# Optimization experiments

Hardware: AMD Instinct MI355X
Metric: run time of the kernel (lower is better)

The kernel has to match this reference:

```python
import jax, jax.numpy as jnp
import numpy as np

DIM = 512; E = 4; K = 4; R = 4; N = 1
B = 32; H = 14; W = 14; TOPK = 2; AUXW = 0.01

def _silu(x):
    return x * jax.nn.sigmoid(x)

def _ss2d(x, in_proj_w, conv_w, conv_b, x_proj_w, dt_proj_w, dt_proj_b, A_logs, Ds, norm_w, norm_b):
    # x: [B,H,W,dim]; single SS2D expert (ssm_ratio=1 -> d_inner=dim), no out_proj, with out_norm
    Bn, Hh, Ww, d = x.shape
    L = Hh * Ww
    xz = jnp.einsum('bhwc,oc->bhwo', x, in_proj_w)            # [B,H,W,2d]
    xp, z = jnp.split(xz, 2, axis=-1)
    xc = xp.transpose(0, 3, 1, 2)                              # [B,d,H,W]
    xc = jax.lax.conv_general_dilated(xc, conv_w, (1, 1), 'SAME', feature_group_count=d)
    xc = _silu(xc + conv_b[None, :, None, None])
    x_hw = xc.reshape(Bn, d, L)
    x_wh = xc.transpose(0, 1, 3, 2).reshape(Bn, d, L)
    # directions: h, h_flip, v, v_flip
    xs = jnp.stack([x_hw, jnp.flip(x_hw, -1), x_wh, jnp.flip(x_wh, -1)], axis=1)  # [B,K,d,L]
    x_dbl = jnp.einsum('bkdl,kcd->bkcl', xs, x_proj_w)         # [B,K,R+2N,L]
    dts = x_dbl[:, :, :R]
    Bs = x_dbl[:, :, R:R + N]                                  # [B,K,N,L]
    Cs = x_dbl[:, :, R + N:]                                   # [B,K,N,L]
    dts = jnp.einsum('bkrl,kdr->bkdl', dts, dt_proj_w)
    dts = jax.nn.softplus(dts + dt_proj_b[None, :, :, None])   # [B,K,d,L]
    A = -jnp.exp(A_logs).reshape(K, d, N)                      # [K,d,N]
    dA = jnp.exp(dts[..., None] * A[None, :, :, None, :])      # [B,K,d,L,N]
    dBu = (dts * xs)[..., None] * Bs.transpose(0, 1, 3, 2)[:, :, None]  # [B,K,d,L,N]
    dA_t = jnp.moveaxis(dA, 3, 0)                              # [L,B,K,d,N]
    dBu_t = jnp.moveaxis(dBu, 3, 0)
    h0 = jnp.zeros((Bn, K, d, N), dtype=x.dtype)
    def step(h, inp):
        a, bu = inp
        h = a * h + bu
        return h, h
    _, hs = jax.lax.scan(step, h0, (dA_t, dBu_t))              # [L,B,K,d,N]
    Cs_t = jnp.moveaxis(Cs, 3, 0)[:, :, :, None, :]            # [L,B,K,1,N]
    y = jnp.moveaxis((hs * Cs_t).sum(-1), 0, -1)               # [B,K,d,L]
    y = y + xs * Ds.reshape(K, d)[None, :, :, None]
    y0 = y[:, 0]
    y1 = jnp.flip(y[:, 1], -1)
    y2 = y[:, 2].reshape(Bn, d, Ww, Hh).transpose(0, 1, 3, 2).reshape(Bn, d, L)
    y3 = jnp.flip(y[:, 3], -1).reshape(Bn, d, Ww, Hh).transpose(0, 1, 3, 2).reshape(Bn, d, L)
    ys = (y0 + y1 + y2 + y3).transpose(0, 2, 1).reshape(Bn, Hh, Ww, d)
    mu = ys.mean(-1, keepdims=True)
    var = ys.var(-1, keepdims=True)
    ys = (ys - mu) * jax.lax.rsqrt(var + 1e-5) * norm_w + norm_b
    return ys * _silu(z)

def setup_inputs() -> dict:
    ks = jax.random.split(jax.random.key(0), 8)
    f = jnp.float32
    return {
        'x': jax.random.normal(ks[0], (B, H, W, DIM), dtype=f),
        'expert_queries': jax.random.normal(ks[1], (E, DIM), dtype=f) / jnp.sqrt(float(DIM)),
        'temperature': jnp.ones((1,), dtype=f),
        'in_proj_w': jax.random.normal(ks[2], (E, 2 * DIM, DIM), dtype=f) / jnp.sqrt(float(DIM)),
        'conv_w': jax.random.normal(ks[3], (E, DIM, 1, 3, 3), dtype=f) / 3.0,
        'conv_b': jnp.zeros((E, DIM), dtype=f),
        'x_proj_w': jax.random.normal(ks[4], (E, K, R + 2 * N, DIM), dtype=f) / jnp.sqrt(float(DIM)),
        'dt_proj_w': jax.random.normal(ks[5], (E, K, DIM, R), dtype=f) / jnp.sqrt(float(R)),
        'dt_proj_b': jnp.zeros((E, K, DIM), dtype=f),
        'A_logs': jax.random.uniform(ks[6], (E, K * DIM, N), dtype=f),
        'Ds': jnp.ones((E, K * DIM), dtype=f),
        'norm_w': jnp.ones((E, DIM), dtype=f),
        'norm_b': jnp.zeros((E, DIM), dtype=f),
    }

def reference(x, expert_queries, temperature, in_proj_w, conv_w, conv_b, x_proj_w, dt_proj_w, dt_proj_b, A_logs, Ds, norm_w, norm_b):
    # spatial gating
    logits = jnp.einsum('bhwd,ed->bhwe', x, expert_queries) / temperature[0]
    gate = jax.nn.softmax(logits, axis=-1)                     # [B,H,W,E]
    avg = gate.mean(axis=(0, 1, 2))
    tk_s, tk_i = jax.lax.top_k(gate, TOPK)                     # [B,H,W,TOPK]
    oh = jax.nn.one_hot(tk_i, E, dtype=gate.dtype)             # [B,H,W,TOPK,E]
    load = (oh.sum(-2) / TOPK).reshape(-1, E).mean(0)
    aux_loss = AUXW * (avg * load).mean() * (E ** 2)
    wts = tk_s / tk_s.sum(-1, keepdims=True)
    comb = (oh * wts[..., None]).sum(-2)                       # [B,H,W,E] scatter of top-k weights
    # dense all-expert SS2D
    eo = jax.vmap(_ss2d, in_axes=(None, 0, 0, 0, 0, 0, 0, 0, 0, 0, 0))(
        x, in_proj_w, conv_w, conv_b, x_proj_w, dt_proj_w, dt_proj_b, A_logs, Ds, norm_w, norm_b)  # [E,B,H,W,dim]
    mixed = jnp.einsum('ebhwc,bhwe->bhwc', eo, comb)
    out = mixed.mean(axis=(1, 2))                              # adaptive_avg_pool2d -> [B,dim]
    return out, aux_loss
```

## Files before the change

### kernel.cpp

```cpp
#include <hip/hip_runtime.h>
#include <math.h>

#define NTOK 6272

typedef __attribute__((ext_vector_type(8))) short short8;
typedef __attribute__((ext_vector_type(8))) unsigned short ushort8;
typedef __attribute__((ext_vector_type(4))) float f32x4;

__device__ __forceinline__ float sigmoidf_(float v){ return 1.0f/(1.0f + expf(-v)); }

__device__ __forceinline__ unsigned short f2b(float f){
  union { float f; unsigned u; } v; v.f = f;
  unsigned r = (v.u + 0x7fffu + ((v.u>>16)&1u)) >> 16;
  return (unsigned short)r;
}

__global__ __launch_bounds__(256) void cvt_bf16_kernel(
    const float* __restrict__ src, unsigned short* __restrict__ dst, int n8)
{
  int i = blockIdx.x*256 + threadIdx.x;
  int stride = gridDim.x*256;
  for (; i < n8; i += stride){
    float4 a = *(const float4*)(src + (size_t)i*8);
    float4 b = *(const float4*)(src + (size_t)i*8 + 4);
    ushort8 o;
    o[0]=f2b(a.x); o[1]=f2b(a.y); o[2]=f2b(a.z); o[3]=f2b(a.w);
    o[4]=f2b(b.x); o[5]=f2b(b.y); o[6]=f2b(b.z); o[7]=f2b(b.w);
    *(ushort8*)(dst + (size_t)i*8) = o;
  }
}

__global__ __launch_bounds__(256) void gate_kernel(
    const float* __restrict__ x, const float* __restrict__ eq,
    const float* __restrict__ temp, float* __restrict__ comb,
    float* __restrict__ avgsum, float* __restrict__ loadsum)
{
  __shared__ float lacc[8];
  if (threadIdx.x < 8) lacc[threadIdx.x] = 0.f;
  __syncthreads();
  int wid = threadIdx.x >> 6, lane = threadIdx.x & 63;
  int m = blockIdx.x*4 + wid;
  const float* xr = x + (size_t)m*512;
  float a0=0.f,a1=0.f,a2=0.f,a3=0.f;
  #pragma unroll
  for (int j=0;j<8;++j){
    float xv = xr[j*64+lane];
    a0 = fmaf(xv, eq[0*512 + j*64+lane], a0);
    a1 = fmaf(xv, eq[1*512 + j*64+lane], a1);
    a2 = fmaf(xv, eq[2*512 + j*64+lane], a2);
    a3 = fmaf(xv, eq[3*512 + j*64+lane], a3);
  }
  #pragma unroll
  for (int off=32; off; off>>=1){
    a0 += __shfl_xor(a0,off); a1 += __shfl_xor(a1,off);
    a2 += __shfl_xor(a2,off); a3 += __shfl_xor(a3,off);
  }
  if (lane == 0){
    float T = temp[0];
    float l0=a0/T, l1=a1/T, l2=a2/T, l3=a3/T;
    float mx = fmaxf(fmaxf(l0,l1), fmaxf(l2,l3));
    float e0=expf(l0-mx), e1=expf(l1-mx), e2=expf(l2-mx), e3=expf(l3-mx);
    float s = e0+e1+e2+e3;
    float g0=e0/s, g1=e1/s, g2=e2/s, g3=e3/s;
    int i1=0; float v1=g0;
    if (g1>v1){v1=g1;i1=1;}
    if (g2>v1){v1=g2;i1=2;}
    if (g3>v1){v1=g3;i1=3;}
    int i2=-1; float v2=-2.f;
    if (i1!=0)          {v2=g0;i2=0;}
    if (i1!=1 && g1>v2) {v2=g1;i2=1;}
    if (i1!=2 && g2>v2) {v2=g2;i2=2;}
    if (i1!=3 && g3>v2) {v2=g3;i2=3;}
    float inv = 1.f/(v1+v2);
    float c0 = (i1==0)? v1*inv : ((i2==0)? v2*inv : 0.f);
    float c1 = (i1==1)? v1*inv : ((i2==1)? v2*inv : 0.f);
    float c2 = (i1==2)? v1*inv : ((i2==2)? v2*inv : 0.f);
    float c3 = (i1==3)? v1*inv : ((i2==3)? v2*inv : 0.f);
    comb[(size_t)m*4+0]=c0; comb[(size_t)m*4+1]=c1;
    comb[(size_t)m*4+2]=c2; comb[(size_t)m*4+3]=c3;
    atomicAdd(&lacc[0], g0); atomicAdd(&lacc[1], g1);
    atomicAdd(&lacc[2], g2); atomicAdd(&lacc[3], g3);
    atomicAdd(&lacc[4+i1], 0.5f);
    atomicAdd(&lacc[4+i2], 0.5f);
  }
  __syncthreads();
  if (threadIdx.x < 4){
    atomicAdd(&avgsum[threadIdx.x],  lacc[threadIdx.x]);
    atomicAdd(&loadsum[threadIdx.x], lacc[4+threadIdx.x]);
  }
}

__global__ void aux_kernel(const float* __restrict__ avgsum,
                           const float* __restrict__ loadsum,
                           float* __restrict__ out_aux)
{
  if (threadIdx.x == 0 && blockIdx.x == 0){
    float s = 0.f;
    #pragma unroll
    for (int e=0;e<4;++e)
      s += (avgsum[e]/(float)NTOK) * (loadsum[e]/(float)NTOK);
    out_aux[0] = 0.01f * (s * 0.25f) * 16.0f;
  }
}

__global__ __launch_bounds__(256) void gemm_bf16(
    const unsigned short* __restrict__ A, const unsigned short* __restrict__ W,
    float* __restrict__ C)
{
  __shared__ unsigned short As[128][56];
  __shared__ unsigned short Bs[128][56];
  const unsigned short* We = W + (size_t)blockIdx.z*524288;
  float* Ce = C + (size_t)blockIdx.z*6422528;
  int m0 = blockIdx.x*128, n0 = blockIdx.y*128;
  int t = threadIdx.x;
  int srow = t>>1, scol = (t&1)*16;
  int w = t>>6, lane = t&63;
  int wr = (w>>1)*64, wc = (w&1)*64;
  int fr = lane&15, fk = (lane>>4)*8;
  f32x4 acc[4][4] = {};
  const unsigned short* ap = A  + (size_t)(m0+srow)*512 + scol;
  const unsigned short* bp = We + (size_t)(n0+srow)*512 + scol;
  for (int k0=0; k0<512; k0+=32){
    ushort8 va0 = *(const ushort8*)(ap+k0);
    ushort8 va1 = *(const ushort8*)(ap+k0+8);
    ushort8 vb0 = *(const ushort8*)(bp+k0);
    ushort8 vb1 = *(const ushort8*)(bp+k0+8);
    __syncthreads();
    *(ushort8*)&As[srow][scol]   = va0;
    *(ushort8*)&As[srow][scol+8] = va1;
    *(ushort8*)&Bs[srow][scol]   = vb0;
    *(ushort8*)&Bs[srow][scol+8] = vb1;
    __syncthreads();
    short8 af[4], bf[4];
    #pragma unroll
    for (int i=0;i<4;++i){
      af[i] = *(short8*)&As[wr+i*16+fr][fk];
      bf[i] = *(short8*)&Bs[wc+i*16+fr][fk];
    }
    #pragma unroll
    for (int i=0;i<4;++i)
      #pragma unroll
      for (int j=0;j<4;++j)
        acc[i][j] = __builtin_amdgcn_mfma_f32_16x16x32_bf16(af[i],bf[j],acc[i][j],0,0,0);
  }
  int orow = (lane>>4)*4;
  #pragma unroll
  for (int i=0;i<4;++i)
    #pragma unroll
    for (int j=0;j<4;++j)
      #pragma unroll
      for (int r=0;r<4;++r)
        Ce[(size_t)(m0+wr+i*16+orow+r)*1024 + n0+wc+j*16+fr] = acc[i][j][r];
}

__global__ __launch_bounds__(256) void gemm_mfma(
    const float* __restrict__ A, const float* __restrict__ W,
    float* __restrict__ C, size_t wStride, size_t cStride)
{
  __shared__ unsigned short As[64][56];
  __shared__ unsigned short Bs[64][56];
  const float* We = W + (size_t)blockIdx.z*wStride;
  float* Ce = C + (size_t)blockIdx.z*cStride;
  int m0 = blockIdx.x*64, n0 = blockIdx.y*64;
  int t = threadIdx.x;
  int srow = t>>2, scol = (t&3)*8;
  int w = t>>6, lane = t&63;
  int wr = (w>>1)*32, wc = (w&1)*32;
  int fr = lane&15, fk = (lane>>4)*8;
  f32x4 acc00={0.f,0.f,0.f,0.f}, acc01={0.f,0.f,0.f,0.f};
  f32x4 acc10={0.f,0.f,0.f,0.f}, acc11={0.f,0.f,0.f,0.f};
  const float* ap = A  + (size_t)(m0+srow)*512 + scol;
  const float* bp = We + (size_t)(n0+srow)*512 + scol;
  for (int k0=0; k0<512; k0+=32){
    float4 av0 = *(const float4*)(ap+k0);
    float4 av1 = *(const float4*)(ap+k0+4);
    float4 bv0 = *(const float4*)(bp+k0);
    float4 bv1 = *(const float4*)(bp+k0+4);
    ushort8 va, vb;
    va[0]=f2b(av0.x); va[1]=f2b(av0.y); va[2]=f2b(av0.z); va[3]=f2b(av0.w);
    va[4]=f2b(av1.x); va[5]=f2b(av1.y); va[6]=f2b(av1.z); va[7]=f2b(av1.w);
    vb[0]=f2b(bv0.x); vb[1]=f2b(bv0.y); vb[2]=f2b(bv0.z); vb[3]=f2b(bv0.w);
    vb[4]=f2b(bv1.x); vb[5]=f2b(bv1.y); vb[6]=f2b(bv1.z); vb[7]=f2b(bv1.w);
    __syncthreads();
    *(ushort8*)&As[srow][scol] = va;
    *(ushort8*)&Bs[srow][scol] = vb;
    __syncthreads();
    short8 a0 = *(short8*)&As[wr+fr][fk];
    short8 a1 = *(short8*)&As[wr+16+fr][fk];
    short8 b0 = *(short8*)&Bs[wc+fr][fk];
    short8 b1 = *(short8*)&Bs[wc+16+fr][fk];
    acc00 = __builtin_amdgcn_mfma_f32_16x16x32_bf16(a0,b0,acc00,0,0,0);
    acc01 = __builtin_amdgcn_mfma_f32_16x16x32_bf16(a0,b1,acc01,0,0,0);
    acc10 = __builtin_amdgcn_mfma_f32_16x16x32_bf16(a1,b0,acc10,0,0,0);
    acc11 = __builtin_amdgcn_mfma_f32_16x16x32_bf16(a1,b1,acc11,0,0,0);
  }
  int orow = (lane>>4)*4;
  #pragma unroll
  for (int r=0;r<4;++r){
    Ce[(size_t)(m0+wr+orow+r)*1024    + n0+wc+fr]    = acc00[r];
    Ce[(size_t)(m0+wr+orow+r)*1024    + n0+wc+16+fr] = acc01[r];
    Ce[(size_t)(m0+wr+16+orow+r)*1024 + n0+wc+fr]    = acc10[r];
    Ce[(size_t)(m0+wr+16+orow+r)*1024 + n0+wc+16+fr] = acc11[r];
  }
}

__global__ __launch_bounds__(512) void convproj_kernel(
    const float* __restrict__ xz, const float* __restrict__ cw,
    const float* __restrict__ cb, const float* __restrict__ xw,
    float* __restrict__ xc, float* __restrict__ proj,
    size_t xzS, size_t xcS, size_t prS)
{
  __shared__ float sact[512];
  int chunk = gridDim.x >> 3;
  int bid = blockIdx.x;
  int flat = (bid & 7)*chunk + (bid >> 3);
  int h  = flat % 14;
  int be = flat / 14;
  int b  = be & 31;
  int e  = be >> 5;
  const float* xze = xz + (size_t)e*xzS;
  const float* cwe = cw + (size_t)e*4608;
  const float* xwe = xw + (size_t)e*12288;
  float* xce = xc + (size_t)e*xcS;
  float* pre = proj + (size_t)e*prS;
  int d = threadIdx.x;
  int wv = d>>6, lane = d&63;
  int d0 = lane*8;

  float wreg[9];
  #pragma unroll
  for (int i=0;i<9;++i) wreg[i] = cwe[d*9+i];
  float bias = cb[(size_t)e*512 + d];

  const float* base = xze + ((size_t)b*196 + (size_t)h*14)*1024 + d;

  for (int w=0; w<14; ++w){
    float s = bias;
    #pragma unroll
    for (int dh=-1; dh<=1; ++dh){
      int hh = h+dh; if ((unsigned)hh >= 14u) continue;
      #pragma unroll
      for (int dw=-1; dw<=1; ++dw){
        int ww = w+dw; if ((unsigned)ww >= 14u) continue;
        s = fmaf(base[(ptrdiff_t)(dh*14 + ww)*1024], wreg[(dh+1)*3 + (dw+1)], s);
      }
    }
    float sa = s * sigmoidf_(s);
    size_t m = (size_t)b*196 + h*14 + w;
    xce[m*512 + d] = sa;
    __syncthreads();
    sact[d] = sa;
    __syncthreads();
    float4 v0 = *(const float4*)&sact[d0];
    float4 v1 = *(const float4*)&sact[d0+4];
    #pragma unroll
    for (int j=0;j<3;++j){
      int kc = wv*3 + j;
      const float* wr = xwe + (size_t)kc*512 + d0;
      float4 w0 = *(const float4*)(wr);
      float4 w1 = *(const float4*)(wr+4);
      float a = v0.x*w0.x + v0.y*w0.y + v0.z*w0.z + v0.w*w0.w
              + v1.x*w1.x + v1.y*w1.y + v1.z*w1.z + v1.w*w1.w;
      #pragma unroll
      for (int off=32; off; off>>=1) a += __shfl_xor(a,off);
      if (lane==0) pre[m*24 + kc] = a;
    }
  }
}

#define WRAP(v) ((v) > 195 ? (v)-195 : ((v) < 0 ? (v)+195 : (v)))

__global__ __launch_bounds__(256) void scan_kernel(
    const float* __restrict__ xc, const float* __restrict__ proj,
    const float* __restrict__ Alogs, const float* __restrict__ Dsp,
    const float* __restrict__ dtw, const float* __restrict__ dtb,
    float* __restrict__ ycomb,
    size_t xcS, size_t prS, size_t ycS)
{
  const float LN2 = 0.6931471805599453f;
  int g = blockIdx.x*256 + threadIdx.x;
  int e  = g >> 16;
  int ge = g & 65535;
  int d = ge & 511;
  int k = (ge >> 9) & 3;
  int b = ge >> 11;
  const float* xce = xc + (size_t)e*xcS;
  const float* pre = proj + (size_t)e*prS;
  float* yce = ycomb + (size_t)e*ycS;
  int eo = e*2048;
  float Ak  = -__expf(Alogs[eo + k*512 + d]);
  float Dk  = Dsp[eo + k*512 + d];
  float btk = dtb[eo + k*512 + d];
  const float* wr = dtw + (size_t)e*8192 + ((size_t)(k*512 + d))*4;
  float w0=wr[0], w1=wr[1], w2=wr[2], w3=wr[3];
  float hst = 0.f;
  const float* xcb = xce + (size_t)b*196*512 + d;
  const float* pb  = pre + (size_t)b*196*24 + k*6;
  float* yb = yce + (size_t)b*196*512 + d;

  int step = (k==0)? 1 : (k==1)? -1 : (k==2)? 14 : -14;
  int t0   = (k==0 || k==2)? 0 : 195;

  int ta=t0, tb_=WRAP(ta+step), tc=WRAP(tb_+step), td_=WRAP(tc+step);
  float  xa=xcb[ta*512],  xb=xcb[tb_*512],  xcv=xcb[tc*512],  xd=xcb[td_*512];
  float2 a0=*(const float2*)(pb+ta*24),  a1=*(const float2*)(pb+ta*24+2),  a2=*(const float2*)(pb+ta*24+4);
  float2 b0=*(const float2*)(pb+tb_*24), b1=*(const float2*)(pb+tb_*24+2), b2=*(const float2*)(pb+tb_*24+4);
  float2 c0=*(const float2*)(pb+tc*24),  c1=*(const float2*)(pb+tc*24+2),  c2=*(const float2*)(pb+tc*24+4);
  float2 d0=*(const float2*)(pb+td_*24), d1=*(const float2*)(pb+td_*24+2), d2=*(const float2*)(pb+td_*24+4);

#define STEP(tt, xv, f0, f1, f2)                                              \
  {                                                                           \
    float dtraw = btk + w0*f0.x + w1*f0.y + w2*f1.x + w3*f1.y;                \
    float sp = fmaxf(dtraw, 0.f) + LN2*__log2f(1.0f + __expf(-fabsf(dtraw))); \
    float dA = __expf(sp*Ak);                                                 \
    hst = fmaf(dA, hst, sp*xv*f2.x);                                          \
    float y = fmaf(hst, f2.y, xv*Dk);                                         \
    atomicAdd(&yb[(tt)*512], y);                                              \
  }

  for (int gg=0; gg<48; ++gg){
    int na = WRAP(td_+step), nb = WRAP(na+step), nc = WRAP(nb+step), nd = WRAP(nc+step);
    float  nxa=xcb[na*512], nxb=xcb[nb*512], nxc=xcb[nc*512], nxd=xcb[nd*512];
    float2 qa0=*(const float2*)(pb+na*24), qa1=*(const float2*)(pb+na*24+2), qa2=*(const float2*)(pb+na*24+4);
    float2 qb0=*(const float2*)(pb+nb*24), qb1=*(const float2*)(pb+nb*24+2), qb2=*(const float2*)(pb+nb*24+4);
    float2 qc0=*(const float2*)(pb+nc*24), qc1=*(const float2*)(pb+nc*24+2), qc2=*(const float2*)(pb+nc*24+4);
    float2 qd0=*(const float2*)(pb+nd*24), qd1=*(const float2*)(pb+nd*24+2), qd2=*(const float2*)(pb+nd*24+4);

    STEP(ta, xa, a0, a1, a2)
    STEP(tb_, xb, b0, b1, b2)
    STEP(tc, xcv, c0, c1, c2)
    STEP(td_, xd, d0, d1, d2)

    ta=na; tb_=nb; tc=nc; td_=nd;
    xa=nxa; xb=nxb; xcv=nxc; xd=nxd;
    a0=qa0; a1=qa1; a2=qa2;
    b0=qb0; b1=qb1; b2=qb2;
    c0=qc0; c1=qc1; c2=qc2;
    d0=qd0; d1=qd1; d2=qd2;
  }
  STEP(ta, xa, a0, a1, a2)
  STEP(tb_, xb, b0, b1, b2)
  STEP(tc, xcv, c0, c1, c2)
  STEP(td_, xd, d0, d1, d2)
#undef STEP
}

template<int NEXP>
__global__ __launch_bounds__(256) void final_kernel(
    const float* __restrict__ ycomb, size_t ycS,
    const float* __restrict__ xz, size_t xzS,
    const float* __restrict__ comb, const float* __restrict__ nw,
    const float* __restrict__ nb, float* __restrict__ out, int e0)
{
  int b = blockIdx.x;
  int wv = threadIdx.x>>6, lane = threadIdx.x&63;
  int t = blockIdx.y*4 + wv;
  size_t tok = (size_t)b*196 + t;
  int d0 = lane*8;
  float acc[8] = {0.f,0.f,0.f,0.f,0.f,0.f,0.f,0.f};
  #pragma unroll
  for (int i=0;i<NEXP;++i){
    const float* yp = ycomb + (size_t)i*ycS + tok*512 + d0;
    float4 y0 = *(const float4*)(yp);
    float4 y1 = *(const float4*)(yp+4);
    float s = y0.x+y0.y+y0.z+y0.w + y1.x+y1.y+y1.z+y1.w;
    float q = y0.x*y0.x+y0.y*y0.y+y0.z*y0.z+y0.w*y0.w
            + y1.x*y1.x+y1.y*y1.y+y1.z*y1.z+y1.w*y1.w;
    #pragma unroll
    for (int off=32; off; off>>=1){ s += __shfl_xor(s,off); q += __shfl_xor(q,off); }
    float mu  = s*(1.f/512.f);
    float var = fmaf(q, (1.f/512.f), -mu*mu);
    float rs  = rsqrtf(var + 1e-5f);
    const float* zp = xz + (size_t)i*xzS + tok*1024 + 512 + d0;
    float4 z0 = *(const float4*)(zp);
    float4 z1 = *(const float4*)(zp+4);
    const float* wp = nw + (size_t)(e0+i)*512 + d0;
    const float* bp = nb + (size_t)(e0+i)*512 + d0;
    float4 w0v = *(const float4*)(wp), w1v = *(const float4*)(wp+4);
    float4 b0v = *(const float4*)(bp), b1v = *(const float4*)(bp+4);
    float cb = comb[tok*4 + e0 + i];
    float yv[8] = {y0.x,y0.y,y0.z,y0.w,y1.x,y1.y,y1.z,y1.w};
    float zv[8] = {z0.x,z0.y,z0.z,z0.w,z1.x,z1.y,z1.z,z1.w};
    float wvv[8]= {w0v.x,w0v.y,w0v.z,w0v.w,w1v.x,w1v.y,w1v.z,w1v.w};
    float bvv[8]= {b0v.x,b0v.y,b0v.z,b0v.w,b1v.x,b1v.y,b1v.z,b1v.w};
    #pragma unroll
    for (int j=0;j<8;++j){
      float ln = (yv[j]-mu)*rs*wvv[j] + bvv[j];
      acc[j] = fmaf(cb*ln, zv[j]*sigmoidf_(zv[j]), acc[j]);
    }
  }
  #pragma unroll
  for (int j=0;j<8;++j)
    atomicAdd(&out[(size_t)b*512 + d0 + j], acc[j]*(1.f/196.f));
}

extern "C" void kernel_launch(void* const* d_in, const int* in_sizes, int n_in,
                              void* d_out, int out_size, void* d_ws, size_t ws_size,
                              hipStream_t stream)
{
  const float* x    = (const float*)d_in[0];
  const float* eq   = (const float*)d_in[1];
  const float* temp = (const float*)d_in[2];
  const float* ipw  = (const float*)d_in[3];
  const float* cw   = (const float*)d_in[4];
  const float* cb   = (const float*)d_in[5];
  const float* xpw  = (const float*)d_in[6];
  const float* dtw  = (const float*)d_in[7];
  const float* dtb  = (const float*)d_in[8];
  const float* alog = (const float*)d_in[9];
  const float* dsp  = (const float*)d_in[10];
  const float* nw   = (const float*)d_in[11];
  const float* nb   = (const float*)d_in[12];
  float* out = (float*)d_out;

  float* ws      = (float*)d_ws;
  float* comb    = ws;
  float* avgsum  = ws + 25088;
  float* loadsum = ws + 25092;

  (void)hipMemsetAsync(avgsum, 0, 8*sizeof(float), stream);
  (void)hipMemsetAsync(d_out, 0, (size_t)out_size*sizeof(float), stream);

  gate_kernel<<<dim3(1568), dim3(256), 0, stream>>>(x, eq, temp, comb, avgsum, loadsum);
  aux_kernel<<<dim3(1), dim3(64), 0, stream>>>(avgsum, loadsum, out + 16384);

  const size_t T2 = 52007936ull;
  const size_t T1 = T2 + 1605632ull + 1048576ull;

  if (ws_size >= T1 * sizeof(float)){
    float* xz = ws + 25600;
    float* xc = xz + 25690112;
    float* pj = xc + 12845056;
    float* yc = pj + 602112;
    unsigned short* xb = (unsigned short*)(yc + 12845056);
    unsigned short* wb = xb + 3211264;
    cvt_bf16_kernel<<<dim3(512), dim3(256), 0, stream>>>(x,   xb, 401408);
    cvt_bf16_kernel<<<dim3(512), dim3(256), 0, stream>>>(ipw, wb, 262144);
    gemm_bf16<<<dim3(49,8,4), dim3(256), 0, stream>>>(xb, wb, xz);
    convproj_kernel<<<dim3(1792), dim3(512), 0, stream>>>(xz, cw, cb, xpw, xc, pj,
                                                          6422528, 3211264, 150528);
    (void)hipMemsetAsync(yc, 0, 12845056ull*sizeof(float), stream);
    scan_kernel<<<dim3(1024), dim3(256), 0, stream>>>(xc, pj, alog, dsp, dtw, dtb, yc,
                                                      3211264, 150528, 3211264);
    final_kernel<4><<<dim3(32,49), dim3(256), 0, stream>>>(yc, 3211264, xz, 6422528,
                                                           comb, nw, nb, out, 0);
  } else if (ws_size >= T2 * sizeof(float)){
    float* xz = ws + 25600;
    float* xc = xz + 25690112;
    float* pj = xc + 12845056;
    float* yc = pj + 602112;
    gemm_mfma<<<dim3(98,16,4), dim3(256), 0, stream>>>(x, ipw, xz, 524288, 6422528);
    convproj_kernel<<<dim3(1792), dim3(512), 0, stream>>>(xz, cw, cb, xpw, xc, pj,
                                                          6422528, 3211264, 150528);
    (void)hipMemsetAsync(yc, 0, 12845056ull*sizeof(float), stream);
    scan_kernel<<<dim3(1024), dim3(256), 0, stream>>>(xc, pj, alog, dsp, dtw, dtb, yc,
                                                      3211264, 150528, 3211264);
    final_kernel<4><<<dim3(32,49), dim3(256), 0, stream>>>(yc, 3211264, xz, 6422528,
                                                           comb, nw, nb, out, 0);
  } else {
    float* xz = ws + 25600;
    float* xc = xz + 6422528;
    float* pj = xc + 3211264;
    float* yc = pj + 150528;
    for (int e=0; e<4; ++e){
      gemm_mfma<<<dim3(98,16,1), dim3(256), 0, stream>>>(x, ipw + (size_t)e*524288, xz, 0, 0);
      convproj_kernel<<<dim3(448), dim3(512), 0, stream>>>(xz, cw + (size_t)e*4608,
          cb + (size_t)e*512, xpw + (size_t)e*12288, xc, pj, 0, 0, 0);
      (void)hipMemsetAsync(yc, 0, 3211264ull*sizeof(float), stream);
      scan_kernel<<<dim3(256), dim3(256), 0, stream>>>(xc, pj,
          alog + (size_t)e*2048, dsp + (size_t)e*2048,
          dtw + (size_t)e*8192, dtb + (size_t)e*2048, yc, 0, 0, 0);
      final_kernel<1><<<dim3(32,49), dim3(256), 0, stream>>>(yc, 0, xz, 0, comb, nw, nb, out, e);
    }
  }
}
```

Before: 531.7 us.

## Write per-direction scan outputs to separate buffers instead of atomic accumulation

Adds a new top workspace tier in which the selective scan writes each direction's output to its own buffer with plain stores, and the final kernel sums the four directions before the layer norm. This removes the atomicAdd contention and the memset of the accumulation buffer. The cost is four times the scan output storage, which must be written and then read back. The fallback scan paths lose their 4-step software pipelining and become a simple loop that prefetches one step ahead.

```diff
diff --git a/kernel.cpp b/kernel.cpp
--- a/kernel.cpp
+++ b/kernel.cpp
@@ -270,12 +270,83 @@
 
 #define WRAP(v) ((v) > 195 ? (v)-195 : ((v) < 0 ? (v)+195 : (v)))
 
-__global__ __launch_bounds__(256) void scan_kernel(
+__global__ __launch_bounds__(256) void scan_split(
     const float* __restrict__ xc, const float* __restrict__ proj,
     const float* __restrict__ Alogs, const float* __restrict__ Dsp,
     const float* __restrict__ dtw, const float* __restrict__ dtb,
-    float* __restrict__ ycomb,
-    size_t xcS, size_t prS, size_t ycS)
+    float* __restrict__ ydir, size_t xcS, size_t prS)
+{
+  const float LN2 = 0.6931471805599453f;
+  int g = blockIdx.x*256 + threadIdx.x;
+  int e  = g >> 16;
+  int ge = g & 65535;
+  int d = ge & 511;
+  int k = (ge >> 9) & 3;
+  int b = ge >> 11;
+  const float* xce = xc + (size_t)e*xcS;
+  const float* pre = proj + (size_t)e*prS;
+  int eo = e*2048;
+  float Ak  = -__expf(Alogs[eo + k*512 + d]);
+  float Dk  = Dsp[eo + k*512 + d];
+  float btk = dtb[eo + k*512 + d];
+  const float* wr = dtw + (size_t)e*8192 + ((size_t)(k*512 + d))*4;
+  float w0=wr[0], w1=wr[1], w2=wr[2], w3=wr[3];
+  float hst = 0.f;
+  const float* xcb = xce + (size_t)b*196*512 + d;
+  const float* pb  = pre + (size_t)b*196*24 + k*6;
+  float* yb = ydir + ((size_t)(e*4 + k))*3211264 + (size_t)b*196*512 + d;
+
+  int step = (k==0)? 1 : (k==1)? -1 : (k==2)? 14 : -14;
+  int t0   = (k==0 || k==2)? 0 : 195;
+
+  int ta=t0, tb_=WRAP(ta+step), tc=WRAP(tb_+step), td_=WRAP(tc+step);
+  float  xa=xcb[ta*512],  xb=xcb[tb_*512],  xcv=xcb[tc*512],  xd=xcb[td_*512];
+  float2 a0=*(const float2*)(pb+ta*24),  a1=*(const float2*)(pb+ta*24+2),  a2=*(const float2*)(pb+ta*24+4);
+  float2 b0=*(const float2*)(pb+tb_*24), b1=*(const float2*)(pb+tb_*24+2), b2=*(const float2*)(pb+tb_*24+4);
+  float2 c0=*(const float2*)(pb+tc*24),  c1=*(const float2*)(pb+tc*24+2),  c2=*(const float2*)(pb+tc*24+4);
+  float2 d0=*(const float2*)(pb+td_*24), d1=*(const float2*)(pb+td_*24+2), d2=*(const float2*)(pb+td_*24+4);
+
+#define STEP(tt, xv, f0, f1, f2)                                              \
+  {                                                                           \
+    float dtraw = btk + w0*f0.x + w1*f0.y + w2*f1.x + w3*f1.y;                \
+    float sp = fmaxf(dtraw, 0.f) + LN2*__log2f(1.0f + __expf(-fabsf(dtraw))); \
+    float dA = __expf(sp*Ak);                                                 \
+    hst = fmaf(dA, hst, sp*xv*f2.x);                                          \
+    yb[(tt)*512] = fmaf(hst, f2.y, xv*Dk);                                    \
+  }
+
+  for (int gg=0; gg<48; ++gg){
+    int na = WRAP(td_+step), nb = WRAP(na+step), nc = WRAP(nb+step), nd = WRAP(nc+step);
+    float  nxa=xcb[na*512], nxb=xcb[nb*512], nxc=xcb[nc*512], nxd=xcb[nd*512];
+    float2 qa0=*(const float2*)(pb+na*24), qa1=*(const float2*)(pb+na*24+2), qa2=*(const float2*)(pb+na*24+4);
+    float2 qb0=*(const float2*)(pb+nb*24), qb1=*(const float2*)(pb+nb*24+2), qb2=*(const float2*)(pb+nb*24+4);
+    float2 qc0=*(const float2*)(pb+nc*24), qc1=*(const float2*)(pb+nc*24+2), qc2=*(const float2*)(pb+nc*24+4);
+    float2 qd0=*(const float2*)(pb+nd*24), qd1=*(const float2*)(pb+nd*24+2), qd2=*(const float2*)(pb+nd*24+4);
+
+    STEP(ta, xa, a0, a1, a2)
+    STEP(tb_, xb, b0, b1, b2)
+    STEP(tc, xcv, c0, c1, c2)
+    STEP(td_, xd, d0, d1, d2)
+
+    ta=na; tb_=nb; tc=nc; td_=nd;
+    xa=nxa; xb=nxb; xcv=nxc; xd=nxd;
+    a0=qa0; a1=qa1; a2=qa2;
+    b0=qb0; b1=qb1; b2=qb2;
+    c0=qc0; c1=qc1; c2=qc2;
+    d0=qd0; d1=qd1; d2=qd2;
+  }
+  STEP(ta, xa, a0, a1, a2)
+  STEP(tb_, xb, b0, b1, b2)
+  STEP(tc, xcv, c0, c1, c2)
+  STEP(td_, xd, d0, d1, d2)
+#undef STEP
+}
+
+__global__ __launch_bounds__(256) void scan_atomic(
+    const float* __restrict__ xc, const float* __restrict__ proj,
+    const float* __restrict__ Alogs, const float* __restrict__ Dsp,
+    const float* __restrict__ dtw, const float* __restrict__ dtb,
+    float* __restrict__ ycomb, size_t xcS, size_t prS, size_t ycS)
 {
   const float LN2 = 0.6931471805599453f;
   int g = blockIdx.x*256 + threadIdx.x;
@@ -299,55 +370,30 @@
   float* yb = yce + (size_t)b*196*512 + d;
 
   int step = (k==0)? 1 : (k==1)? -1 : (k==2)? 14 : -14;
-  int t0   = (k==0 || k==2)? 0 : 195;
-
-  int ta=t0, tb_=WRAP(ta+step), tc=WRAP(tb_+step), td_=WRAP(tc+step);
-  float  xa=xcb[ta*512],  xb=xcb[tb_*512],  xcv=xcb[tc*512],  xd=xcb[td_*512];
-  float2 a0=*(const float2*)(pb+ta*24),  a1=*(const float2*)(pb+ta*24+2),  a2=*(const float2*)(pb+ta*24+4);
-  float2 b0=*(const float2*)(pb+tb_*24), b1=*(const float2*)(pb+tb_*24+2), b2=*(const float2*)(pb+tb_*24+4);
-  float2 c0=*(const float2*)(pb+tc*24),  c1=*(const float2*)(pb+tc*24+2),  c2=*(const float2*)(pb+tc*24+4);
-  float2 d0=*(const float2*)(pb+td_*24), d1=*(const float2*)(pb+td_*24+2), d2=*(const float2*)(pb+td_*24+4);
-
-#define STEP(tt, xv, f0, f1, f2)                                              \
-  {                                                                           \
-    float dtraw = btk + w0*f0.x + w1*f0.y + w2*f1.x + w3*f1.y;                \
-    float sp = fmaxf(dtraw, 0.f) + LN2*__log2f(1.0f + __expf(-fabsf(dtraw))); \
-    float dA = __expf(sp*Ak);                                                 \
-    hst = fmaf(dA, hst, sp*xv*f2.x);                                          \
-    float y = fmaf(hst, f2.y, xv*Dk);                                         \
-    atomicAdd(&yb[(tt)*512], y);                                              \
-  }
-
-  for (int gg=0; gg<48; ++gg){
-    int na = WRAP(td_+step), nb = WRAP(na+step), nc = WRAP(nb+step), nd = WRAP(nc+step);
-    float  nxa=xcb[na*512], nxb=xcb[nb*512], nxc=xcb[nc*512], nxd=xcb[nd*512];
-    float2 qa0=*(const float2*)(pb+na*24), qa1=*(const float2*)(pb+na*24+2), qa2=*(const float2*)(pb+na*24+4);
-    float2 qb0=*(const float2*)(pb+nb*24), qb1=*(const float2*)(pb+nb*24+2), qb2=*(const float2*)(pb+nb*24+4);
-    float2 qc0=*(const float2*)(pb+nc*24), qc1=*(const float2*)(pb+nc*24+2), qc2=*(const float2*)(pb+nc*24+4);
-    float2 qd0=*(const float2*)(pb+nd*24), qd1=*(const float2*)(pb+nd*24+2), qd2=*(const float2*)(pb+nd*24+4);
-
-    STEP(ta, xa, a0, a1, a2)
-    STEP(tb_, xb, b0, b1, b2)
-    STEP(tc, xcv, c0, c1, c2)
-    STEP(td_, xd, d0, d1, d2)
-
-    ta=na; tb_=nb; tc=nc; td_=nd;
-    xa=nxa; xb=nxb; xcv=nxc; xd=nxd;
-    a0=qa0; a1=qa1; a2=qa2;
-    b0=qb0; b1=qb1; b2=qb2;
-    c0=qc0; c1=qc1; c2=qc2;
-    d0=qd0; d1=qd1; d2=qd2;
-  }
-  STEP(ta, xa, a0, a1, a2)
-  STEP(tb_, xb, b0, b1, b2)
-  STEP(tc, xcv, c0, c1, c2)
-  STEP(td_, xd, d0, d1, d2)
-#undef STEP
-}
-
-template<int NEXP>
+  int t = (k==0 || k==2)? 0 : 195;
+  float xval = xcb[t*512];
+  const float* pp = pb + t*24;
+  float p0=pp[0], p1=pp[1], p2=pp[2], p3=pp[3], Bsv=pp[4], Csv=pp[5];
+
+  for (int l=0; l<196; ++l){
+    int tn = WRAP(t + step);
+    float xval_n = xcb[tn*512];
+    const float* ppn = pb + tn*24;
+    float q0=ppn[0], q1=ppn[1], q2=ppn[2], q3=ppn[3], Bn_=ppn[4], Cn_=ppn[5];
+    float dtraw = btk + w0*p0 + w1*p1 + w2*p2 + w3*p3;
+    float sp = fmaxf(dtraw, 0.f) + LN2*__log2f(1.0f + __expf(-fabsf(dtraw)));
+    float dA = __expf(sp*Ak);
+    hst = fmaf(dA, hst, sp*xval*Bsv);
+    float y = fmaf(hst, Csv, xval*Dk);
+    atomicAdd(&yb[t*512], y);
+    t = tn; xval = xval_n;
+    p0=q0; p1=q1; p2=q2; p3=q3; Bsv=Bn_; Csv=Cn_;
+  }
+}
+
+template<int NEXP, int NDIR>
 __global__ __launch_bounds__(256) void final_kernel(
-    const float* __restrict__ ycomb, size_t ycS,
+    const float* __restrict__ ycomb, size_t eS, size_t kS,
     const float* __restrict__ xz, size_t xzS,
     const float* __restrict__ comb, const float* __restrict__ nw,
     const float* __restrict__ nb, float* __restrict__ out, int e0)
@@ -360,12 +406,18 @@
   float acc[8] = {0.f,0.f,0.f,0.f,0.f,0.f,0.f,0.f};
   #pragma unroll
   for (int i=0;i<NEXP;++i){
-    const float* yp = ycomb + (size_t)i*ycS + tok*512 + d0;
-    float4 y0 = *(const float4*)(yp);
-    float4 y1 = *(const float4*)(yp+4);
-    float s = y0.x+y0.y+y0.z+y0.w + y1.x+y1.y+y1.z+y1.w;
-    float q = y0.x*y0.x+y0.y*y0.y+y0.z*y0.z+y0.w*y0.w
-            + y1.x*y1.x+y1.y*y1.y+y1.z*y1.z+y1.w*y1.w;
+    float yv[8] = {0.f,0.f,0.f,0.f,0.f,0.f,0.f,0.f};
+    #pragma unroll
+    for (int kk=0;kk<NDIR;++kk){
+      const float* yp = ycomb + (size_t)i*eS + (size_t)kk*kS + tok*512 + d0;
+      float4 y0 = *(const float4*)(yp);
+      float4 y1 = *(const float4*)(yp+4);
+      yv[0]+=y0.x; yv[1]+=y0.y; yv[2]+=y0.z; yv[3]+=y0.w;
+      yv[4]+=y1.x; yv[5]+=y1.y; yv[6]+=y1.z; yv[7]+=y1.w;
+    }
+    float s=0.f, q=0.f;
+    #pragma unroll
+    for (int j=0;j<8;++j){ s += yv[j]; q += yv[j]*yv[j]; }
     #pragma unroll
     for (int off=32; off; off>>=1){ s += __shfl_xor(s,off); q += __shfl_xor(q,off); }
     float mu  = s*(1.f/512.f);
@@ -378,15 +430,14 @@
     const float* bp = nb + (size_t)(e0+i)*512 + d0;
     float4 w0v = *(const float4*)(wp), w1v = *(const float4*)(wp+4);
     float4 b0v = *(const float4*)(bp), b1v = *(const float4*)(bp+4);
-    float cb = comb[tok*4 + e0 + i];
-    float yv[8] = {y0.x,y0.y,y0.z,y0.w,y1.x,y1.y,y1.z,y1.w};
+    float cbv = comb[tok*4 + e0 + i];
     float zv[8] = {z0.x,z0.y,z0.z,z0.w,z1.x,z1.y,z1.z,z1.w};
     float wvv[8]= {w0v.x,w0v.y,w0v.z,w0v.w,w1v.x,w1v.y,w1v.z,w1v.w};
     float bvv[8]= {b0v.x,b0v.y,b0v.z,b0v.w,b1v.x,b1v.y,b1v.z,b1v.w};
     #pragma unroll
     for (int j=0;j<8;++j){
       float ln = (yv[j]-mu)*rs*wvv[j] + bvv[j];
-      acc[j] = fmaf(cb*ln, zv[j]*sigmoidf_(zv[j]), acc[j]);
+      acc[j] = fmaf(cbv*ln, zv[j]*sigmoidf_(zv[j]), acc[j]);
     }
   }
   #pragma unroll
@@ -426,8 +477,25 @@
 
   const size_t T2 = 52007936ull;
   const size_t T1 = T2 + 1605632ull + 1048576ull;
-
-  if (ws_size >= T1 * sizeof(float)){
+  const size_t T0 = T1 + 38535168ull;
+
+  if (ws_size >= T0 * sizeof(float)){
+    float* xz   = ws + 25600;
+    float* xc   = xz + 25690112;
+    float* pj   = xc + 12845056;
+    float* ydir = pj + 602112;
+    unsigned short* xb = (unsigned short*)(ydir + 51380224);
+    unsigned short* wb = xb + 3211264;
+    cvt_bf16_kernel<<<dim3(512), dim3(256), 0, stream>>>(x,   xb, 401408);
+    cvt_bf16_kernel<<<dim3(512), dim3(256), 0, stream>>>(ipw, wb, 262144);
+    gemm_bf16<<<dim3(49,8,4), dim3(256), 0, stream>>>(xb, wb, xz);
+    convproj_kernel<<<dim3(1792), dim3(512), 0, stream>>>(xz, cw, cb, xpw, xc, pj,
+                                                          6422528, 3211264, 150528);
+    scan_split<<<dim3(1024), dim3(256), 0, stream>>>(xc, pj, alog, dsp, dtw, dtb, ydir,
+                                                     3211264, 150528);
+    final_kernel<4,4><<<dim3(32,49), dim3(256), 0, stream>>>(ydir, 12845056, 3211264,
+                                                             xz, 6422528, comb, nw, nb, out, 0);
+  } else if (ws_size >= T1 * sizeof(float)){
     float* xz = ws + 25600;
     float* xc = xz + 25690112;
     float* pj = xc + 12845056;
@@ -440,10 +508,10 @@
     convproj_kernel<<<dim3(1792), dim3(512), 0, stream>>>(xz, cw, cb, xpw, xc, pj,
                                                           6422528, 3211264, 150528);
     (void)hipMemsetAsync(yc, 0, 12845056ull*sizeof(float), stream);
-    scan_kernel<<<dim3(1024), dim3(256), 0, stream>>>(xc, pj, alog, dsp, dtw, dtb, yc,
+    scan_atomic<<<dim3(1024), dim3(256), 0, stream>>>(xc, pj, alog, dsp, dtw, dtb, yc,
                                                       3211264, 150528, 3211264);
-    final_kernel<4><<<dim3(32,49), dim3(256), 0, stream>>>(yc, 3211264, xz, 6422528,
-                                                           comb, nw, nb, out, 0);
+    final_kernel<4,1><<<dim3(32,49), dim3(256), 0, stream>>>(yc, 3211264, 0,
+                                                             xz, 6422528, comb, nw, nb, out, 0);
   } else if (ws_size >= T2 * sizeof(float)){
     float* xz = ws + 25600;
     float* xc = xz + 25690112;
@@ -453,10 +521,10 @@
     convproj_kernel<<<dim3(1792), dim3(512), 0, stream>>>(xz, cw, cb, xpw, xc, pj,
                                                           6422528, 3211264, 150528);
     (void)hipMemsetAsync(yc, 0, 12845056ull*sizeof(float), stream);
-    scan_kernel<<<dim3(1024), dim3(256), 0, stream>>>(xc, pj, alog, dsp, dtw, dtb, yc,
+    scan_atomic<<<dim3(1024), dim3(256), 0, stream>>>(xc, pj, alog, dsp, dtw, dtb, yc,
                                                       3211264, 150528, 3211264);
-    final_kernel<4><<<dim3(32,49), dim3(256), 0, stream>>>(yc, 3211264, xz, 6422528,
-                                                           comb, nw, nb, out, 0);
+    final_kernel<4,1><<<dim3(32,49), dim3(256), 0, stream>>>(yc, 3211264, 0,
+                                                             xz, 6422528, comb, nw, nb, out, 0);
   } else {
     float* xz = ws + 25600;
     float* xc = xz + 6422528;
@@ -467,10 +535,11 @@
       convproj_kernel<<<dim3(448), dim3(512), 0, stream>>>(xz, cw + (size_t)e*4608,
           cb + (size_t)e*512, xpw + (size_t)e*12288, xc, pj, 0, 0, 0);
       (void)hipMemsetAsync(yc, 0, 3211264ull*sizeof(float), stream);
-      scan_kernel<<<dim3(256), dim3(256), 0, stream>>>(xc, pj,
+      scan_atomic<<<dim3(256), dim3(256), 0, stream>>>(xc, pj,
           alog + (size_t)e*2048, dsp + (size_t)e*2048,
           dtw + (size_t)e*8192, dtb + (size_t)e*2048, yc, 0, 0, 0);
-      final_kernel<1><<<dim3(32,49), dim3(256), 0, stream>>>(yc, 0, xz, 0, comb, nw, nb, out, e);
+      final_kernel<1,1><<<dim3(32,49), dim3(256), 0, stream>>>(yc, 0, 0, xz, 0,
+                                                               comb, nw, nb, out, e);
     }
   }
 }
```

Result: no change. 527.4 us (-0.8%).
